# Optimization experiments

Hardware: AMD Instinct MI355X
Metric: run time of the kernel (lower is better)

Reference implementation:

```python
import jax, jax.numpy as jnp
import numpy as np

T, H, E, K = 16384, 2880, 128, 4

def setup_inputs() -> dict:
    key = jax.random.key(0)
    k1, k2, k3 = jax.random.split(key, 3)
    return {
        "hidden_states": jax.random.normal(k1, (T, H), dtype=jnp.float32),
        "weight": jax.random.normal(k2, (E, H), dtype=jnp.float32) * 0.02,
        "bias": jax.random.normal(k3, (E,), dtype=jnp.float32) * 0.02,
    }

def reference(hidden_states, weight, bias):
    x = hidden_states.reshape(-1, weight.shape[1])            # [T, H]
    logits = jnp.einsum('th,eh->te', x, weight) + bias        # [T, E]
    top_val, top_idx = jax.lax.top_k(logits, K)               # sorted desc, [T, K]
    top_val = jax.nn.softmax(top_val, axis=-1)
    rows = jnp.arange(logits.shape[0])[:, None]
    scores = jnp.zeros_like(logits).at[rows, top_idx].set(top_val)
    return scores, top_idx
```

## Files before the change

### kernel.cpp

```cpp
#include <hip/hip_runtime.h>
#include <math.h>


#define T_TOK 16384
#define HDIM  2880
#define EEXP  128
#define KTOP  4

#define TM    64
#define NT    512
#define KC    32
#define NCH   (HDIM / KC)
#define ROWS  (TM + EEXP)
#define RB    128
#define BUFB  (ROWS * RB)
#define TAU   2.5e-4f

typedef __attribute__((ext_vector_type(8))) short bf16x8;
typedef __attribute__((ext_vector_type(4))) float f32x4;

static __device__ __forceinline__ void split_write(char* base, int off, float4 v) {
    union { float4 v4; unsigned u[4]; } uv; uv.v4 = v;
    unsigned h01 = __builtin_amdgcn_perm(uv.u[1], uv.u[0], 0x07060302u);
    unsigned h23 = __builtin_amdgcn_perm(uv.u[3], uv.u[2], 0x07060302u);
    float r0 = v.x - __uint_as_float(uv.u[0] & 0xffff0000u);
    float r1 = v.y - __uint_as_float(uv.u[1] & 0xffff0000u);
    float r2 = v.z - __uint_as_float(uv.u[2] & 0xffff0000u);
    float r3 = v.w - __uint_as_float(uv.u[3] & 0xffff0000u);
    unsigned l01 = __builtin_amdgcn_perm(__float_as_uint(r1), __float_as_uint(r0), 0x07060302u);
    unsigned l23 = __builtin_amdgcn_perm(__float_as_uint(r3), __float_as_uint(r2), 0x07060302u);
    uint2 hw; hw.x = h01; hw.y = h23;
    uint2 lw; lw.x = l01; lw.y = l23;
    *(uint2*)(base + off)        = hw;
    *(uint2*)(base + (off ^ 64)) = lw;
}

#define MFMA_OP __builtin_amdgcn_mfma_f32_16x16x32_bf16

__global__ __launch_bounds__(NT, 2) void router_fused(
    const float* __restrict__ x, const float* __restrict__ w,
    const float* __restrict__ bias, float* __restrict__ out)
{
    __shared__ char smem[2 * BUFB];
    const int tid  = threadIdx.x;
    const int tok0 = blockIdx.x * TM;
    const int lane = tid & 63;
    const int wv   = tid >> 6;
    const int wt   = wv & 1;
    const int wn   = wv >> 1;
    const int r    = lane & 15;
    const int g    = lane >> 4;

    const float* sptr[3];
    int soff[3];
#pragma unroll
    for (int i = 0; i < 3; ++i) {
        int f = tid + i * NT;
        int row = f >> 3, c4 = f & 7;
        soff[i] = row * RB + ((((c4 >> 1) ^ (row & 7)) << 4) | ((c4 & 1) << 3));
        sptr[i] = (row < TM) ? (x + (size_t)(tok0 + row) * HDIM + c4 * 4)
                             : (w + (size_t)(row - TM) * HDIM + c4 * 4);
    }

    const int ar0 = wt * 32 + r,      ar1 = wt * 32 + 16 + r;
    const int br0 = TM + wn * 32 + r, br1 = TM + wn * 32 + 16 + r;
    const int aH0 = ar0 * RB + ((g ^ (ar0 & 7)) << 4);
    const int aH1 = ar1 * RB + ((g ^ (ar1 & 7)) << 4);
    const int bH0 = br0 * RB + ((g ^ (br0 & 7)) << 4);
    const int bH1 = br1 * RB + ((g ^ (br1 & 7)) << 4);

    f32x4 a00 = {0.f,0.f,0.f,0.f}, a01 = a00, a10 = a00, a11 = a00;

#define DO_MFMA(cb) do {                                            \
        bf16x8 ah0 = *(const bf16x8*)((cb) + aH0);                  \
        bf16x8 al0 = *(const bf16x8*)((cb) + (aH0 ^ 64));           \
        bf16x8 ah1 = *(const bf16x8*)((cb) + aH1);                  \
        bf16x8 al1 = *(const bf16x8*)((cb) + (aH1 ^ 64));           \
        bf16x8 bh0 = *(const bf16x8*)((cb) + bH0);                  \
        bf16x8 bl0 = *(const bf16x8*)((cb) + (bH0 ^ 64));           \
        bf16x8 bh1 = *(const bf16x8*)((cb) + bH1);                  \
        bf16x8 bl1 = *(const bf16x8*)((cb) + (bH1 ^ 64));           \
        a00 = MFMA_OP(ah0, bh0, a00, 0, 0, 0);                      \
        a01 = MFMA_OP(ah0, bh1, a01, 0, 0, 0);                      \
        a10 = MFMA_OP(ah1, bh0, a10, 0, 0, 0);                      \
        a11 = MFMA_OP(ah1, bh1, a11, 0, 0, 0);                      \
        a00 = MFMA_OP(ah0, bl0, a00, 0, 0, 0);                      \
        a01 = MFMA_OP(ah0, bl1, a01, 0, 0, 0);                      \
        a10 = MFMA_OP(ah1, bl0, a10, 0, 0, 0);                      \
        a11 = MFMA_OP(ah1, bl1, a11, 0, 0, 0);                      \
        a00 = MFMA_OP(al0, bh0, a00, 0, 0, 0);                      \
        a01 = MFMA_OP(al0, bh1, a01, 0, 0, 0);                      \
        a10 = MFMA_OP(al1, bh0, a10, 0, 0, 0);                      \
        a11 = MFMA_OP(al1, bh1, a11, 0, 0, 0);                      \
    } while (0)

#define LOADS(pf, ch) do { int k0_ = (ch) * KC;                     \
        pf[0] = *(const float4*)(sptr[0] + k0_);                    \
        pf[1] = *(const float4*)(sptr[1] + k0_);                    \
        pf[2] = *(const float4*)(sptr[2] + k0_); } while (0)

#define WRITES(pf, bb) do {                                         \
        split_write((bb), soff[0], pf[0]);                          \
        split_write((bb), soff[1], pf[1]);                          \
        split_write((bb), soff[2], pf[2]); } while (0)

    char* b0 = smem;
    char* b1 = smem + BUFB;
    float4 pfA[3], pfB[3];

    LOADS(pfA, 0);
    LOADS(pfB, 1);
    WRITES(pfA, b0);
    __syncthreads();

    for (int c = 0; c < NCH; c += 2) {
        if (c + 2 < NCH) LOADS(pfA, c + 2);
        DO_MFMA(b0);
        WRITES(pfB, b1);
        __syncthreads();
        if (c + 3 < NCH) LOADS(pfB, c + 3);
        DO_MFMA(b1);
        if (c + 2 < NCH) WRITES(pfA, b0);
        __syncthreads();
    }

    float* logitsL = (float*)smem;
    const float bv0 = bias[wn * 32 + r];
    const float bv1 = bias[wn * 32 + 16 + r];
#pragma unroll
    for (int q = 0; q < 4; ++q) {
        int m0 = wt * 32 + g * 4 + q, m1 = m0 + 16;
        int e0 = wn * 32 + r,         e1 = e0 + 16;
        logitsL[m0 * 130 + e0] = a00[q] + bv0;
        logitsL[m0 * 130 + e1] = a01[q] + bv1;
        logitsL[m1 * 130 + e0] = a10[q] + bv0;
        logitsL[m1 * 130 + e1] = a11[q] + bv1;
    }

    float*  cvf = (float*) (smem + 33280);
    int*    cie = (int*)   (smem + 35328);
    int*    flg = (int*)   (smem + 37376);
    double* svd = (double*)(smem + 37632);
    int*    sid = (int*)   (smem + 39680);
    double* cvd = (double*)(smem + 40704);
    __syncthreads();

    {
        const int t = tid >> 3, s = tid & 7;
        float v[8]; int id[8];
#pragma unroll
        for (int k = 0; k < 8; ++k) { v[k] = -3.4e38f; id[k] = 0x7fffffff; }
        for (int jj = 0; jj < 16; ++jj) {
            float lv = logitsL[t * 130 + s * 16 + jj];
            int   e  = s * 16 + jj;
            bool gt[8];
#pragma unroll
            for (int k = 0; k < 8; ++k)
                gt[k] = (lv > v[k]) || (lv == v[k] && e < id[k]);
#pragma unroll
            for (int k = 7; k >= 1; --k)
                if (gt[k - 1]) { v[k] = v[k - 1]; id[k] = id[k - 1]; }
#pragma unroll
            for (int k = 0; k < 8; ++k) {
                bool put = gt[k] && (k == 0 || !gt[k - 1]);
                if (put) { v[k] = lv; id[k] = e; }
            }
        }
#pragma unroll
        for (int rd = 0; rd < 8; ++rd) {
            float hv = v[0]; int hi = id[0];
#pragma unroll
            for (int off = 1; off < 8; off <<= 1) {
                float ov = __shfl_xor(hv, off);
                int   oi = __shfl_xor(hi, off);
                if (ov > hv || (ov == hv && oi < hi)) { hv = ov; hi = oi; }
            }
            if (s == 0) { cvf[t * 8 + rd] = hv; cie[t * 8 + rd] = hi; }
            bool mine = (v[0] == hv) && (id[0] == hi);
            if (mine) {
#pragma unroll
                for (int k = 0; k < 7; ++k) { v[k] = v[k + 1]; id[k] = id[k + 1]; }
                v[7] = -3.4e38f; id[7] = 0x7fffffff;
            }
        }
    }
    __syncthreads();

    if (tid < TM) {
        float gmin = 3.4e38f;
#pragma unroll
        for (int k = 0; k < 4; ++k)
            gmin = fminf(gmin, cvf[tid * 8 + k] - cvf[tid * 8 + k + 1]);
        flg[tid] = (gmin < TAU);
    }
    if (tid < 256) {
        int t2 = tid >> 2, k = tid & 3;
        svd[t2 * 4 + k] = (double)cvf[t2 * 8 + k];
        sid[t2 * 4 + k] = cie[t2 * 8 + k];
    }
    __syncthreads();

    for (int ts = 0; ts < TM; ++ts) {
        if (!flg[ts]) continue;
        const int ce = cie[ts * 8 + wv];
        const float4* xr = (const float4*)(x + (size_t)(tok0 + ts) * HDIM);
        const float4* wr = (const float4*)(w + (size_t)ce * HDIM);
        double q0 = 0.0, q1 = 0.0, q2 = 0.0, q3 = 0.0;
        for (int i2 = 0; i2 < 12; ++i2) {
            int fi = lane + i2 * 64;
            if (fi < HDIM / 4) {
                float4 xv = xr[fi];
                float4 wv4 = wr[fi];
                q0 = fma((double)xv.x, (double)wv4.x, q0);
                q1 = fma((double)xv.y, (double)wv4.y, q1);
                q2 = fma((double)xv.z, (double)wv4.z, q2);
                q3 = fma((double)xv.w, (double)wv4.w, q3);
            }
        }
        double accd = (q0 + q2) + (q1 + q3);
#pragma unroll
        for (int off = 32; off > 0; off >>= 1)
            accd += __shfl_xor(accd, off);
        if (lane == 0) cvd[wv] = accd + (double)bias[ce];
        __syncthreads();
        if (tid < 8) {
            double mv = cvd[tid]; int mi2 = cie[ts * 8 + tid];
            int rk = 0;
#pragma unroll
            for (int j2 = 0; j2 < 8; ++j2) {
                double oj = cvd[j2];
                rk += (oj > mv) || (oj == mv && cie[ts * 8 + j2] < mi2);
            }
            if (rk < 4) { svd[ts * 4 + rk] = mv; sid[ts * 4 + rk] = mi2; }
        }
        __syncthreads();
    }

    float* srow = (float*)smem;
    {
        float4 z4 = make_float4(0.f, 0.f, 0.f, 0.f);
#pragma unroll
        for (int i = 0; i < 4; ++i)
            ((float4*)srow)[tid + i * NT] = z4;
    }
    __syncthreads();

    if (tid < TM) {
        double m  = svd[tid * 4];
        double e0 = exp(svd[tid * 4 + 0] - m), e1 = exp(svd[tid * 4 + 1] - m);
        double e2 = exp(svd[tid * 4 + 2] - m), e3 = exp(svd[tid * 4 + 3] - m);
        double inv = 1.0 / ((e0 + e1) + (e2 + e3));
        float* oidx = out + (size_t)T_TOK * EEXP + (size_t)(tok0 + tid) * KTOP;
        int i0 = sid[tid * 4 + 0], i1 = sid[tid * 4 + 1];
        int i2 = sid[tid * 4 + 2], i3 = sid[tid * 4 + 3];
        oidx[0] = (float)i0; oidx[1] = (float)i1;
        oidx[2] = (float)i2; oidx[3] = (float)i3;
        srow[tid * EEXP + i0] = (float)(e0 * inv);
        srow[tid * EEXP + i1] = (float)(e1 * inv);
        srow[tid * EEXP + i2] = (float)(e2 * inv);
        srow[tid * EEXP + i3] = (float)(e3 * inv);
    }
    __syncthreads();

    float4* orow = (float4*)(out + (size_t)tok0 * EEXP);
#pragma unroll
    for (int i = 0; i < 4; ++i)
        orow[tid + i * NT] = ((float4*)srow)[tid + i * NT];
}

extern "C" void kernel_launch(void* const* d_in, const int* in_sizes, int n_in,
                              void* d_out, int out_size, void* d_ws, size_t ws_size,
                              hipStream_t stream) {
    const float* x    = (const float*)d_in[0];
    const float* w    = (const float*)d_in[1];
    const float* bias = (const float*)d_in[2];
    float* out        = (float*)d_out;

    hipLaunchKernelGGL(router_fused, dim3(T_TOK / TM), dim3(NT), 0, stream,
                       x, w, bias, out);
}
```

Before: 97.09 us.

## Pre-split weights into MFMA-fragment layout and stream them from global per wave

Adds a pre-pass kernel that converts the fp32 router weight into bf16 hi/lo pairs already arranged in MFMA register-fragment order in the workspace. The main kernel then drops weights from shared memory, loading each wave's weight fragments straight into registers, and stages only x in LDS. Tiles shrink to 32 tokens with 256 threads and a 64-wide K chunk. This removes the per-block weight conversion and LDS traffic, but costs an extra launch, more global weight reads (re-fetched per block, likely L2-resident) and more register pressure.

Measured after the change: 85.09 us. 1.14x faster.

```diff
diff --git a/kernel.cpp b/kernel.cpp
--- a/kernel.cpp
+++ b/kernel.cpp
@@ -7,19 +7,49 @@
 #define EEXP  128
 #define KTOP  4
 
-#define TM    64
-#define NT    512
-#define KC    32
-#define NCH   (HDIM / KC)
-#define ROWS  (TM + EEXP)
-#define RB    128
-#define BUFB  (ROWS * RB)
-#define TAU   2.5e-4f
+#define TM   32
+#define NT   256
+#define KC   64
+#define NCH  (HDIM / KC)
+#define XBUF 8192
+#define TAU  2.5e-4f
 
 typedef __attribute__((ext_vector_type(8))) short bf16x8;
 typedef __attribute__((ext_vector_type(4))) float f32x4;
 
-static __device__ __forceinline__ void split_write(char* base, int off, float4 v) {
+#define MFMA(a, b, c) __builtin_amdgcn_mfma_f32_16x16x32_bf16((a), (b), (c), 0, 0, 0)
+
+__global__ __launch_bounds__(256) void w_split(
+    const float* __restrict__ w, char* __restrict__ wp)
+{
+    const int gid  = blockIdx.x * 256 + threadIdx.x;
+    const int lane = gid & 63;
+    const int q    = gid >> 6;
+    const int ks   = q & 1;
+    const int q2   = q >> 1;
+    const int c    = q2 % NCH;
+    const int F    = q2 / NCH;
+    const int e    = F * 16 + (lane & 15);
+    const int k0   = c * 64 + ks * 32 + (lane >> 4) * 8;
+
+    const float* src = w + (size_t)e * HDIM + k0;
+    float4 v0 = *(const float4*)(src);
+    float4 v1 = *(const float4*)(src + 4);
+    float vv[8] = {v0.x, v0.y, v0.z, v0.w, v1.x, v1.y, v1.z, v1.w};
+    union { unsigned short s[8]; uint4 u; } H, L;
+#pragma unroll
+    for (int j = 0; j < 8; ++j) {
+        unsigned u = __float_as_uint(vv[j]);
+        H.s[j] = (unsigned short)(u >> 16);
+        float rr = vv[j] - __uint_as_float(u & 0xffff0000u);
+        L.s[j] = (unsigned short)(__float_as_uint(rr) >> 16);
+    }
+    const int tile = ((F * NCH + c) * 2 + ks) * 2;
+    *(uint4*)(wp + (size_t)tile * 1024 + lane * 16)       = H.u;
+    *(uint4*)(wp + (size_t)(tile + 1) * 1024 + lane * 16) = L.u;
+}
+
+static __device__ __forceinline__ void split_write256(char* base, int off, float4 v) {
     union { float4 v4; unsigned u[4]; } uv; uv.v4 = v;
     unsigned h01 = __builtin_amdgcn_perm(uv.u[1], uv.u[0], 0x07060302u);
     unsigned h23 = __builtin_amdgcn_perm(uv.u[3], uv.u[2], 0x07060302u);
@@ -31,118 +61,122 @@
     unsigned l23 = __builtin_amdgcn_perm(__float_as_uint(r3), __float_as_uint(r2), 0x07060302u);
     uint2 hw; hw.x = h01; hw.y = h23;
     uint2 lw; lw.x = l01; lw.y = l23;
-    *(uint2*)(base + off)        = hw;
-    *(uint2*)(base + (off ^ 64)) = lw;
+    *(uint2*)(base + off)       = hw;
+    *(uint2*)(base + off + 128) = lw;
 }
 
-#define MFMA_OP __builtin_amdgcn_mfma_f32_16x16x32_bf16
-
 __global__ __launch_bounds__(NT, 2) void router_fused(
-    const float* __restrict__ x, const float* __restrict__ w,
-    const float* __restrict__ bias, float* __restrict__ out)
+    const float* __restrict__ x, const char* __restrict__ wp,
+    const float* __restrict__ w, const float* __restrict__ bias,
+    float* __restrict__ out)
 {
-    __shared__ char smem[2 * BUFB];
+    __shared__ char smem[20480];
     const int tid  = threadIdx.x;
     const int tok0 = blockIdx.x * TM;
     const int lane = tid & 63;
     const int wv   = tid >> 6;
-    const int wt   = wv & 1;
-    const int wn   = wv >> 1;
     const int r    = lane & 15;
     const int g    = lane >> 4;
 
-    const float* sptr[3];
-    int soff[3];
-#pragma unroll
-    for (int i = 0; i < 3; ++i) {
+    char* xb0 = smem;
+    char* xb1 = smem + XBUF;
+
+    int xoff[2];
+    const float* xptr[2];
+#pragma unroll
+    for (int i = 0; i < 2; ++i) {
         int f = tid + i * NT;
-        int row = f >> 3, c4 = f & 7;
-        soff[i] = row * RB + ((((c4 >> 1) ^ (row & 7)) << 4) | ((c4 & 1) << 3));
-        sptr[i] = (row < TM) ? (x + (size_t)(tok0 + row) * HDIM + c4 * 4)
-                             : (w + (size_t)(row - TM) * HDIM + c4 * 4);
-    }
-
-    const int ar0 = wt * 32 + r,      ar1 = wt * 32 + 16 + r;
-    const int br0 = TM + wn * 32 + r, br1 = TM + wn * 32 + 16 + r;
-    const int aH0 = ar0 * RB + ((g ^ (ar0 & 7)) << 4);
-    const int aH1 = ar1 * RB + ((g ^ (ar1 & 7)) << 4);
-    const int bH0 = br0 * RB + ((g ^ (br0 & 7)) << 4);
-    const int bH1 = br1 * RB + ((g ^ (br1 & 7)) << 4);
-
-    f32x4 a00 = {0.f,0.f,0.f,0.f}, a01 = a00, a10 = a00, a11 = a00;
-
-#define DO_MFMA(cb) do {                                            \
-        bf16x8 ah0 = *(const bf16x8*)((cb) + aH0);                  \
-        bf16x8 al0 = *(const bf16x8*)((cb) + (aH0 ^ 64));           \
-        bf16x8 ah1 = *(const bf16x8*)((cb) + aH1);                  \
-        bf16x8 al1 = *(const bf16x8*)((cb) + (aH1 ^ 64));           \
-        bf16x8 bh0 = *(const bf16x8*)((cb) + bH0);                  \
-        bf16x8 bl0 = *(const bf16x8*)((cb) + (bH0 ^ 64));           \
-        bf16x8 bh1 = *(const bf16x8*)((cb) + bH1);                  \
-        bf16x8 bl1 = *(const bf16x8*)((cb) + (bH1 ^ 64));           \
-        a00 = MFMA_OP(ah0, bh0, a00, 0, 0, 0);                      \
-        a01 = MFMA_OP(ah0, bh1, a01, 0, 0, 0);                      \
-        a10 = MFMA_OP(ah1, bh0, a10, 0, 0, 0);                      \
-        a11 = MFMA_OP(ah1, bh1, a11, 0, 0, 0);                      \
-        a00 = MFMA_OP(ah0, bl0, a00, 0, 0, 0);                      \
-        a01 = MFMA_OP(ah0, bl1, a01, 0, 0, 0);                      \
-        a10 = MFMA_OP(ah1, bl0, a10, 0, 0, 0);                      \
-        a11 = MFMA_OP(ah1, bl1, a11, 0, 0, 0);                      \
-        a00 = MFMA_OP(al0, bh0, a00, 0, 0, 0);                      \
-        a01 = MFMA_OP(al0, bh1, a01, 0, 0, 0);                      \
-        a10 = MFMA_OP(al1, bh0, a10, 0, 0, 0);                      \
-        a11 = MFMA_OP(al1, bh1, a11, 0, 0, 0);                      \
-    } while (0)
-
-#define LOADS(pf, ch) do { int k0_ = (ch) * KC;                     \
-        pf[0] = *(const float4*)(sptr[0] + k0_);                    \
-        pf[1] = *(const float4*)(sptr[1] + k0_);                    \
-        pf[2] = *(const float4*)(sptr[2] + k0_); } while (0)
-
-#define WRITES(pf, bb) do {                                         \
-        split_write((bb), soff[0], pf[0]);                          \
-        split_write((bb), soff[1], pf[1]);                          \
-        split_write((bb), soff[2], pf[2]); } while (0)
-
-    char* b0 = smem;
-    char* b1 = smem + BUFB;
-    float4 pfA[3], pfB[3];
-
-    LOADS(pfA, 0);
-    LOADS(pfB, 1);
-    WRITES(pfA, b0);
-    __syncthreads();
-
-    for (int c = 0; c < NCH; c += 2) {
-        if (c + 2 < NCH) LOADS(pfA, c + 2);
-        DO_MFMA(b0);
-        WRITES(pfB, b1);
+        int row = f >> 4, c4 = f & 15;
+        xoff[i] = row * 256 + ((((c4 >> 1) ^ (row & 7)) << 4) | ((c4 & 1) << 3));
+        xptr[i] = x + (size_t)(tok0 + row) * HDIM + c4 * 4;
+    }
+
+    int aoff[2][2];
+#pragma unroll
+    for (int tf = 0; tf < 2; ++tf) {
+        int row = tf * 16 + r;
+#pragma unroll
+        for (int ks = 0; ks < 2; ++ks)
+            aoff[tf][ks] = row * 256 + (((ks * 4 + g) ^ (row & 7)) << 4);
+    }
+
+    f32x4 a00 = {0.f, 0.f, 0.f, 0.f}, a01 = a00, a10 = a00, a11 = a00;
+
+#define LOADX(pf, cc) do {                                            \
+        pf[0] = *(const float4*)(xptr[0] + (cc) * KC);                \
+        pf[1] = *(const float4*)(xptr[1] + (cc) * KC); } while (0)
+
+#define WRITEX(pf, bb) do {                                           \
+        split_write256((bb), xoff[0], pf[0]);                         \
+        split_write256((bb), xoff[1], pf[1]); } while (0)
+
+#define LOADW(W, cc) do {                                             \
+        _Pragma("unroll")                                             \
+        for (int F2 = 0; F2 < 2; ++F2)                                \
+        _Pragma("unroll")                                             \
+        for (int ks_ = 0; ks_ < 2; ++ks_)                             \
+        _Pragma("unroll")                                             \
+        for (int p_ = 0; p_ < 2; ++p_)                                \
+            W[F2*4 + ks_*2 + p_] = *(const bf16x8*)(wp +              \
+                (size_t)((((wv*2 + F2) * NCH + (cc)) * 2 + ks_) * 2 + p_) * 1024 \
+                + lane * 16); } while (0)
+
+#define MFMA_CHUNK(cb, W) do {                                        \
+        _Pragma("unroll")                                             \
+        for (int ks_ = 0; ks_ < 2; ++ks_) {                           \
+            bf16x8 ah0 = *(const bf16x8*)((cb) + aoff[0][ks_]);       \
+            bf16x8 al0 = *(const bf16x8*)((cb) + aoff[0][ks_] + 128); \
+            bf16x8 ah1 = *(const bf16x8*)((cb) + aoff[1][ks_]);       \
+            bf16x8 al1 = *(const bf16x8*)((cb) + aoff[1][ks_] + 128); \
+            bf16x8 bh0 = W[ks_*2],     bl0 = W[ks_*2 + 1];            \
+            bf16x8 bh1 = W[4 + ks_*2], bl1 = W[4 + ks_*2 + 1];        \
+            a00 = MFMA(ah0, bh0, a00); a01 = MFMA(ah0, bh1, a01);     \
+            a10 = MFMA(ah1, bh0, a10); a11 = MFMA(ah1, bh1, a11);     \
+            a00 = MFMA(ah0, bl0, a00); a01 = MFMA(ah0, bl1, a01);     \
+            a10 = MFMA(ah1, bl0, a10); a11 = MFMA(ah1, bl1, a11);     \
+            a00 = MFMA(al0, bh0, a00); a01 = MFMA(al0, bh1, a01);     \
+            a10 = MFMA(al1, bh0, a10); a11 = MFMA(al1, bh1, a11);     \
+        } } while (0)
+
+    float4 pf[2];
+    bf16x8 wA[8], wB[8];
+
+    LOADX(pf, 0);
+    LOADW(wA, 0);
+    WRITEX(pf, xb0);
+    __syncthreads();
+
+    for (int c = 0; c < NCH - 1; c += 2) {
+        LOADX(pf, c + 1); LOADW(wB, c + 1);
+        MFMA_CHUNK(xb0, wA);
+        WRITEX(pf, xb1);
         __syncthreads();
-        if (c + 3 < NCH) LOADS(pfB, c + 3);
-        DO_MFMA(b1);
-        if (c + 2 < NCH) WRITES(pfA, b0);
+        if (c + 2 < NCH) { LOADX(pf, c + 2); LOADW(wA, c + 2); }
+        MFMA_CHUNK(xb1, wB);
+        if (c + 2 < NCH) WRITEX(pf, xb0);
         __syncthreads();
     }
+    MFMA_CHUNK(xb0, wA);
+    __syncthreads();
 
     float* logitsL = (float*)smem;
-    const float bv0 = bias[wn * 32 + r];
-    const float bv1 = bias[wn * 32 + 16 + r];
+    const float bv0 = bias[wv * 32 + r];
+    const float bv1 = bias[wv * 32 + 16 + r];
 #pragma unroll
     for (int q = 0; q < 4; ++q) {
-        int m0 = wt * 32 + g * 4 + q, m1 = m0 + 16;
-        int e0 = wn * 32 + r,         e1 = e0 + 16;
+        int m0 = g * 4 + q, m1 = m0 + 16;
+        int e0 = wv * 32 + r, e1 = e0 + 16;
         logitsL[m0 * 130 + e0] = a00[q] + bv0;
         logitsL[m0 * 130 + e1] = a01[q] + bv1;
         logitsL[m1 * 130 + e0] = a10[q] + bv0;
         logitsL[m1 * 130 + e1] = a11[q] + bv1;
     }
-
-    float*  cvf = (float*) (smem + 33280);
-    int*    cie = (int*)   (smem + 35328);
-    int*    flg = (int*)   (smem + 37376);
-    double* svd = (double*)(smem + 37632);
-    int*    sid = (int*)   (smem + 39680);
-    double* cvd = (double*)(smem + 40704);
+    float*  cvf = (float*) (smem + 16640);
+    int*    cie = (int*)   (smem + 17664);
+    int*    flg = (int*)   (smem + 18688);
+    double* svd = (double*)(smem + 18816);
+    int*    sid = (int*)   (smem + 19840);
+    double* cvd = (double*)(smem + 20352);
     __syncthreads();
 
     {
@@ -193,7 +227,7 @@
             gmin = fminf(gmin, cvf[tid * 8 + k] - cvf[tid * 8 + k + 1]);
         flg[tid] = (gmin < TAU);
     }
-    if (tid < 256) {
+    if (tid < 128) {
         int t2 = tid >> 2, k = tid & 3;
         svd[t2 * 4 + k] = (double)cvf[t2 * 8 + k];
         sid[t2 * 4 + k] = cie[t2 * 8 + k];
@@ -202,26 +236,30 @@
 
     for (int ts = 0; ts < TM; ++ts) {
         if (!flg[ts]) continue;
-        const int ce = cie[ts * 8 + wv];
-        const float4* xr = (const float4*)(x + (size_t)(tok0 + ts) * HDIM);
-        const float4* wr = (const float4*)(w + (size_t)ce * HDIM);
-        double q0 = 0.0, q1 = 0.0, q2 = 0.0, q3 = 0.0;
-        for (int i2 = 0; i2 < 12; ++i2) {
-            int fi = lane + i2 * 64;
-            if (fi < HDIM / 4) {
-                float4 xv = xr[fi];
-                float4 wv4 = wr[fi];
-                q0 = fma((double)xv.x, (double)wv4.x, q0);
-                q1 = fma((double)xv.y, (double)wv4.y, q1);
-                q2 = fma((double)xv.z, (double)wv4.z, q2);
-                q3 = fma((double)xv.w, (double)wv4.w, q3);
-            }
+#pragma unroll
+        for (int h2 = 0; h2 < 2; ++h2) {
+            const int cand = wv * 2 + h2;
+            const int ce = cie[ts * 8 + cand];
+            const float4* xr = (const float4*)(x + (size_t)(tok0 + ts) * HDIM);
+            const float4* wr = (const float4*)(w + (size_t)ce * HDIM);
+            double q0 = 0.0, q1 = 0.0, q2 = 0.0, q3 = 0.0;
+            for (int i2 = 0; i2 < 12; ++i2) {
+                int fi = lane + i2 * 64;
+                if (fi < HDIM / 4) {
+                    float4 xv = xr[fi];
+                    float4 wv4 = wr[fi];
+                    q0 = fma((double)xv.x, (double)wv4.x, q0);
+                    q1 = fma((double)xv.y, (double)wv4.y, q1);
+                    q2 = fma((double)xv.z, (double)wv4.z, q2);
+                    q3 = fma((double)xv.w, (double)wv4.w, q3);
+                }
+            }
+            double accd = (q0 + q2) + (q1 + q3);
+#pragma unroll
+            for (int off = 32; off > 0; off >>= 1)
+                accd += __shfl_xor(accd, off);
+            if (lane == 0) cvd[cand] = accd + (double)bias[ce];
         }
-        double accd = (q0 + q2) + (q1 + q3);
-#pragma unroll
-        for (int off = 32; off > 0; off >>= 1)
-            accd += __shfl_xor(accd, off);
-        if (lane == 0) cvd[wv] = accd + (double)bias[ce];
         __syncthreads();
         if (tid < 8) {
             double mv = cvd[tid]; int mi2 = cie[ts * 8 + tid];
@@ -237,12 +275,10 @@
     }
 
     float* srow = (float*)smem;
-    {
-        float4 z4 = make_float4(0.f, 0.f, 0.f, 0.f);
-#pragma unroll
-        for (int i = 0; i < 4; ++i)
-            ((float4*)srow)[tid + i * NT] = z4;
-    }
+    float4 z4 = make_float4(0.f, 0.f, 0.f, 0.f);
+#pragma unroll
+    for (int i = 0; i < 4; ++i)
+        ((float4*)srow)[tid + i * NT] = z4;
     __syncthreads();
 
     if (tid < TM) {
@@ -275,7 +311,9 @@
     const float* w    = (const float*)d_in[1];
     const float* bias = (const float*)d_in[2];
     float* out        = (float*)d_out;
-
+    char*  wp         = (char*)d_ws;
+
+    hipLaunchKernelGGL(w_split, dim3(180), dim3(256), 0, stream, w, wp);
     hipLaunchKernelGGL(router_fused, dim3(T_TOK / TM), dim3(NT), 0, stream,
-                       x, w, bias, out);
+                       x, wp, w, bias, out);
 }
```
